# Kernel tuning notes

Measured on AMD Instinct MI355X. Metric: run time of the kernel, lower is better.

Reference implementation:

```python
import jax, jax.numpy as jnp
import numpy as np

GRID_MIN, GRID_MAX = -3.0, 3.0
N_AXIS = 64            # 64x64 grid -> m = 4096
LENGTHSCALE = 0.5      # RBF kernel lengthscale
EPS = 1e-6


def make_grid():
    lin = jnp.linspace(GRID_MIN, GRID_MAX, N_AXIS, dtype=jnp.float32)
    gx, gy = jnp.meshgrid(lin, lin, indexing='ij')
    return jnp.stack([gx.ravel(), gy.ravel()], axis=-1)  # [m, 2]


def setup_inputs() -> dict:
    key = jax.random.key(0)
    k1, k2 = jax.random.split(key)
    X = jax.random.normal(k1, (16, 1024, 2), dtype=jnp.float32)  # context locations
    Y = jax.random.normal(k2, (16, 1024, 8), dtype=jnp.float32)  # context values
    return {"X": X, "Y": Y}


def reference(X, Y):
    grid = make_grid()                                   # [m, 2]
    # expand_with_ones: prepend a ones channel (density channel)
    ones = jnp.ones(Y.shape[:-1] + (1,), dtype=Y.dtype)
    Yb = jnp.concatenate([ones, Y], axis=-1)             # [b, n, 1+dy]

    # kernel_smooth: RBF kernel between grid and X, contracted with Yb.
    # squared distances via the expanded form (avoids [b,m,n,2] intermediate)
    g2 = jnp.sum(grid * grid, axis=-1)                   # [m]
    x2 = jnp.sum(X * X, axis=-1)                         # [b, n]
    gx = jnp.einsum('md,bnd->bmn', grid, X)              # [b, m, n]
    d2 = g2[None, :, None] + x2[:, None, :] - 2.0 * gx   # [b, m, n]
    K = jnp.exp(-d2 / (2.0 * LENGTHSCALE * LENGTHSCALE)) # [b, m, n]

    Y_grid = jnp.einsum('bmn,bnc->bmc', K, Yb)           # [b, m, 1+dy]

    # normalise: divide feature channels by the density channel
    density = Y_grid[:, :, :1]
    feats = Y_grid[:, :, 1:] / (density + EPS)
    Y_grid = jnp.concatenate([density, feats], axis=-1)

    return grid[None], Y_grid
```

## Files before the change

### kernel.cpp

```cpp
#include <hip/hip_runtime.h>

typedef _Float16 half8   __attribute__((ext_vector_type(8)));
typedef float    floatx4 __attribute__((ext_vector_type(4)));

#define STEP  (6.0f / 63.0f)
#define SCAL  1.69864636f

#define EYF_SZ (16 * 65536)
#define EXF_SZ (16 * 65536)
#define YBF_SZ (16 * 16384)

__global__ __launch_bounds__(256) void rkhs_tables(
    const float* __restrict__ X, const float* __restrict__ Y,
    _Float16* __restrict__ EyF, _Float16* __restrict__ ExF,
    _Float16* __restrict__ YbF)
{
    const int gid = blockIdx.x * 256 + threadIdx.x;
    if (gid < 131072) {
        const int n = gid & 15, q = (gid >> 4) & 3, ct = (gid >> 6) & 3,
                  s = (gid >> 8) & 31, b = gid >> 13;
        const int col = ct * 16 + n, k0 = s * 32 + q * 8;
        const float gS = SCAL * (-3.0f + (float)col * STEP);
        half8 h;
#pragma unroll
        for (int j = 0; j < 8; ++j) {
            const float x = X[(((b << 10) + k0 + j) << 1) + 1];
            const float d = fmaf(-SCAL, x, gS);
            h[j] = (_Float16)__builtin_amdgcn_exp2f(-(d * d));
        }
        *(half8*)(EyF + (size_t)gid * 8) = h;
    } else if (gid < 262144) {
        const int u = gid - 131072;
        const int qq = u & 3, r = (u >> 2) & 63, s = (u >> 8) & 31, b = u >> 13;
        const int k0 = s * 32 + qq * 8;
        const float gS = SCAL * (-3.0f + (float)r * STEP);
        half8 h;
#pragma unroll
        for (int j = 0; j < 8; ++j) {
            const float x = X[(((b << 10) + k0 + j) << 1)];
            const float d = fmaf(-SCAL, x, gS);
            h[j] = (_Float16)__builtin_amdgcn_exp2f(-(d * d));
        }
        *(half8*)(ExF + (size_t)u * 8) = h;
    } else {
        const int v = gid - 262144;
        const int n = v & 15, q = (v >> 4) & 3, s = (v >> 6) & 31, b = v >> 11;
        const int k0 = s * 32 + q * 8;
        half8 h;
#pragma unroll
        for (int j = 0; j < 8; ++j) {
            float val = 0.f;
            if (n == 0)      val = 1.f;
            else if (n <= 8) val = Y[(((b << 10) + k0 + j) << 3) + n - 1];
            h[j] = (_Float16)val;
        }
        *(half8*)(YbF + (size_t)v * 8) = h;
    }
}

__global__ __launch_bounds__(512, 2) void rkhs_gemm(
    const _Float16* __restrict__ EyF, const _Float16* __restrict__ ExF,
    const _Float16* __restrict__ YbF, float* __restrict__ out)
{
    __shared__ float2 red[3][2][16][64];

    const int b   = blockIdx.x >> 4;
    const int rg  = blockIdx.x & 15;
    const int tid = threadIdx.x;
    const int wv  = tid >> 6, l = tid & 63, q = l >> 4, n = l & 15;
    const int kq  = wv & 3, rp = wv >> 2;
    const int r0  = rg * 4 + rp * 2;

    floatx4 acc[2][4];
#pragma unroll
    for (int r = 0; r < 2; ++r)
#pragma unroll
        for (int ct = 0; ct < 4; ++ct) acc[r][ct] = (floatx4){0.f, 0.f, 0.f, 0.f};

#pragma unroll
    for (int ss = 0; ss < 8; ++ss) {
        const int s = kq * 8 + ss;
        const size_t sb = (size_t)(b * 32 + s);
        const half8 yb  = *(const half8*)(YbF + (sb * 64 + l) * 8);
        const half8 ex0 = *(const half8*)(ExF + (sb * 64 + r0) * 32 + q * 8);
        const half8 ex1 = *(const half8*)(ExF + (sb * 64 + r0 + 1) * 32 + q * 8);
        const half8 bp0 = ex0 * yb;
        const half8 bp1 = ex1 * yb;
#pragma unroll
        for (int ct = 0; ct < 4; ++ct) {
            const half8 ey = *(const half8*)(EyF + ((sb * 4 + ct) * 64 + l) * 8);
            acc[0][ct] = __builtin_amdgcn_mfma_f32_16x16x32_f16(ey, bp0, acc[0][ct], 0, 0, 0);
            acc[1][ct] = __builtin_amdgcn_mfma_f32_16x16x32_f16(ey, bp1, acc[1][ct], 0, 0, 0);
        }
    }

    if (kq != 0) {
#pragma unroll
        for (int r = 0; r < 2; ++r)
#pragma unroll
            for (int ct = 0; ct < 4; ++ct)
#pragma unroll
                for (int h = 0; h < 2; ++h)
                    red[kq - 1][rp][(r * 4 + ct) * 2 + h][l] =
                        make_float2(acc[r][ct][2 * h], acc[r][ct][2 * h + 1]);
    }
    __syncthreads();

    if (b == 0) {
        const int p = tid >> 1;
        const int row = rg * 4 + (p >> 6), col = p & 63;
        out[(size_t)rg * 512 + tid] =
            (tid & 1) ? (-3.0f + (float)col * STEP) : (-3.0f + (float)row * STEP);
    }

    if (kq == 0) {
#pragma unroll
        for (int t = 0; t < 3; ++t)
#pragma unroll
            for (int r = 0; r < 2; ++r)
#pragma unroll
                for (int ct = 0; ct < 4; ++ct)
#pragma unroll
                    for (int h = 0; h < 2; ++h) {
                        const float2 v = red[t][rp][(r * 4 + ct) * 2 + h][l];
                        acc[r][ct][2 * h]     += v.x;
                        acc[r][ct][2 * h + 1] += v.y;
                    }
#pragma unroll
        for (int r = 0; r < 2; ++r) {
            const int row = r0 + r;
#pragma unroll
            for (int ct = 0; ct < 4; ++ct)
#pragma unroll
                for (int i = 0; i < 4; ++i) {
                    const float dv  = __shfl(acc[r][ct][i], l & 48);
                    const float inv = __builtin_amdgcn_rcpf(dv + 1e-6f);
                    if (n < 9) {
                        const int m = row * 64 + ct * 16 + q * 4 + i;
                        const float v = acc[r][ct][i];
                        out[8192 + ((size_t)(b << 12) + m) * 9 + n] = n ? v * inv : v;
                    }
                }
        }
    }
}

extern "C" void kernel_launch(void* const* d_in, const int* in_sizes, int n_in,
                              void* d_out, int out_size, void* d_ws, size_t ws_size,
                              hipStream_t stream) {
    const float* X = (const float*)d_in[0];
    const float* Y = (const float*)d_in[1];
    float* out = (float*)d_out;

    _Float16* EyF = (_Float16*)d_ws;
    _Float16* ExF = EyF + EYF_SZ;
    _Float16* YbF = ExF + EXF_SZ;

    rkhs_tables<<<dim3(1152), dim3(256), 0, stream>>>(X, Y, EyF, ExF, YbF);
    rkhs_gemm  <<<dim3(256),  dim3(512), 0, stream>>>(EyF, ExF, YbF, out);
}
```

Before: 69.31 us.

## Split K across all eight waves with tree reduction and coalesced output staging

Each wave now computes all four grid rows of the block over a quarter-sized K slice (4 steps instead of 8), reusing each EyF load across four row MFMAs. The partial sums from the eight waves are combined through LDS in a three-level tree reduction. The final normalised tile is staged in shared memory so that all threads write output contiguously instead of strided per-lane stores. The trade-off is more accumulator registers, more shared memory and several extra barriers.

After: 67.58 us. -2.5%, faster.

```diff
diff --git a/kernel.cpp b/kernel.cpp
--- a/kernel.cpp
+++ b/kernel.cpp
@@ -62,85 +62,93 @@
     const _Float16* __restrict__ EyF, const _Float16* __restrict__ ExF,
     const _Float16* __restrict__ YbF, float* __restrict__ out)
 {
-    __shared__ float2 red[3][2][16][64];
+    __shared__ floatx4 spark[4096];
+    float* sfin = (float*)spark;
 
     const int b   = blockIdx.x >> 4;
-    const int rg  = blockIdx.x & 15;
+    const int rw  = blockIdx.x & 15;
     const int tid = threadIdx.x;
-    const int wv  = tid >> 6, l = tid & 63, q = l >> 4, n = l & 15;
-    const int kq  = wv & 3, rp = wv >> 2;
-    const int r0  = rg * 4 + rp * 2;
+    const int kq  = tid >> 6, l = tid & 63, q = l >> 4, n = l & 15;
+    const int r0  = rw * 4;
 
-    floatx4 acc[2][4];
+    if (b == 0) {
+        const int row = r0 + (tid >> 7), rem = tid & 127;
+        out[(size_t)rw * 512 + tid] = (rem & 1)
+            ? (-3.0f + (float)(rem >> 1) * STEP)
+            : (-3.0f + (float)row * STEP);
+    }
+
+    floatx4 acc[4][4];
 #pragma unroll
-    for (int r = 0; r < 2; ++r)
+    for (int rr = 0; rr < 4; ++rr)
 #pragma unroll
-        for (int ct = 0; ct < 4; ++ct) acc[r][ct] = (floatx4){0.f, 0.f, 0.f, 0.f};
+        for (int ct = 0; ct < 4; ++ct) acc[rr][ct] = (floatx4){0.f, 0.f, 0.f, 0.f};
 
 #pragma unroll
-    for (int ss = 0; ss < 8; ++ss) {
-        const int s = kq * 8 + ss;
+    for (int ss = 0; ss < 4; ++ss) {
+        const int s = kq * 4 + ss;
         const size_t sb = (size_t)(b * 32 + s);
-        const half8 yb  = *(const half8*)(YbF + (sb * 64 + l) * 8);
-        const half8 ex0 = *(const half8*)(ExF + (sb * 64 + r0) * 32 + q * 8);
-        const half8 ex1 = *(const half8*)(ExF + (sb * 64 + r0 + 1) * 32 + q * 8);
-        const half8 bp0 = ex0 * yb;
-        const half8 bp1 = ex1 * yb;
+        const half8 yb = *(const half8*)(YbF + (sb * 64 + l) * 8);
+        half8 bp[4];
+#pragma unroll
+        for (int rr = 0; rr < 4; ++rr) {
+            const half8 ex = *(const half8*)(ExF + (sb * 64 + r0 + rr) * 32 + q * 8);
+            bp[rr] = ex * yb;
+        }
 #pragma unroll
         for (int ct = 0; ct < 4; ++ct) {
             const half8 ey = *(const half8*)(EyF + ((sb * 4 + ct) * 64 + l) * 8);
-            acc[0][ct] = __builtin_amdgcn_mfma_f32_16x16x32_f16(ey, bp0, acc[0][ct], 0, 0, 0);
-            acc[1][ct] = __builtin_amdgcn_mfma_f32_16x16x32_f16(ey, bp1, acc[1][ct], 0, 0, 0);
+#pragma unroll
+            for (int rr = 0; rr < 4; ++rr)
+                acc[rr][ct] = __builtin_amdgcn_mfma_f32_16x16x32_f16(ey, bp[rr], acc[rr][ct], 0, 0, 0);
         }
     }
 
-    if (kq != 0) {
+#define PARKA(slot)                                                        \
+    { _Pragma("unroll") for (int rr = 0; rr < 4; ++rr)                     \
+      _Pragma("unroll") for (int ct = 0; ct < 4; ++ct)                     \
+          spark[(slot) * 1024 + (rr * 4 + ct) * 64 + l] = acc[rr][ct]; }
+#define ABSORBA(slot)                                                      \
+    { _Pragma("unroll") for (int rr = 0; rr < 4; ++rr)                     \
+      _Pragma("unroll") for (int ct = 0; ct < 4; ++ct)                     \
+          acc[rr][ct] += spark[(slot) * 1024 + (rr * 4 + ct) * 64 + l]; }
+
+    if (kq >= 4) PARKA(kq - 4)
+    __syncthreads();
+    if (kq < 4)  ABSORBA(kq)
+    __syncthreads();
+    if (kq == 2 || kq == 3) PARKA(kq - 2)
+    __syncthreads();
+    if (kq < 2)  ABSORBA(kq)
+    __syncthreads();
+    if (kq == 1) PARKA(0)
+    __syncthreads();
+
+    if (kq == 0) {
+        ABSORBA(0)
 #pragma unroll
-        for (int r = 0; r < 2; ++r)
+        for (int rr = 0; rr < 4; ++rr)
 #pragma unroll
             for (int ct = 0; ct < 4; ++ct)
+                if (n < 9)
 #pragma unroll
-                for (int h = 0; h < 2; ++h)
-                    red[kq - 1][rp][(r * 4 + ct) * 2 + h][l] =
-                        make_float2(acc[r][ct][2 * h], acc[r][ct][2 * h + 1]);
+                    for (int i = 0; i < 4; ++i)
+                        sfin[(rr * 64 + ct * 16 + q * 4 + i) * 9 + n] = acc[rr][ct][i];
     }
+#undef PARKA
+#undef ABSORBA
     __syncthreads();
 
-    if (b == 0) {
-        const int p = tid >> 1;
-        const int row = rg * 4 + (p >> 6), col = p & 63;
-        out[(size_t)rg * 512 + tid] =
-            (tid & 1) ? (-3.0f + (float)col * STEP) : (-3.0f + (float)row * STEP);
-    }
-
-    if (kq == 0) {
+    const size_t obase = 8192 + ((size_t)b * 4096 + (size_t)r0 * 64) * 9;
 #pragma unroll
-        for (int t = 0; t < 3; ++t)
-#pragma unroll
-            for (int r = 0; r < 2; ++r)
-#pragma unroll
-                for (int ct = 0; ct < 4; ++ct)
-#pragma unroll
-                    for (int h = 0; h < 2; ++h) {
-                        const float2 v = red[t][rp][(r * 4 + ct) * 2 + h][l];
-                        acc[r][ct][2 * h]     += v.x;
-                        acc[r][ct][2 * h + 1] += v.y;
-                    }
-#pragma unroll
-        for (int r = 0; r < 2; ++r) {
-            const int row = r0 + r;
-#pragma unroll
-            for (int ct = 0; ct < 4; ++ct)
-#pragma unroll
-                for (int i = 0; i < 4; ++i) {
-                    const float dv  = __shfl(acc[r][ct][i], l & 48);
-                    const float inv = __builtin_amdgcn_rcpf(dv + 1e-6f);
-                    if (n < 9) {
-                        const int m = row * 64 + ct * 16 + q * 4 + i;
-                        const float v = acc[r][ct][i];
-                        out[8192 + ((size_t)(b << 12) + m) * 9 + n] = n ? v * inv : v;
-                    }
-                }
+    for (int it = 0; it < 5; ++it) {
+        const int idx = it * 512 + tid;
+        if (idx < 2304) {
+            const int m  = idx / 9;
+            const int ch = idx - m * 9;
+            const float dens = sfin[m * 9];
+            const float v    = sfin[idx];
+            out[obase + idx] = ch ? v * __builtin_amdgcn_rcpf(dens + 1e-6f) : dens;
         }
     }
 }
```
